# Kernel optimization log

Measured on AMD Instinct MI355X. Metric: run time of the kernel, lower is better.

Reference implementation:

```python
import jax, jax.numpy as jnp
import numpy as np

B, C, T = 128, 295, 2048
D1 = 270
NUM_SUBJECTS = 64

def setup_inputs() -> dict:
    key = jax.random.key(0)
    k_x, k_s, k_w1, k_b1, k_ws = jax.random.split(key, 5)
    X = jax.random.normal(k_x, (B, C, T), dtype=jnp.float32)
    subject_idxs = jax.random.randint(k_s, (B,), 0, NUM_SUBJECTS)
    W1 = jax.random.normal(k_w1, (D1, C), dtype=jnp.float32) * 0.05
    b1 = jax.random.normal(k_b1, (D1,), dtype=jnp.float32) * 0.05
    Ws = jax.random.normal(k_ws, (NUM_SUBJECTS, D1, D1), dtype=jnp.float32) * 0.05
    return {"X": X, "subject_idxs": subject_idxs, "W1": W1, "b1": b1, "Ws": Ws}

def reference(X, subject_idxs, W1, b1, Ws):
    # Shared 1x1 conv: pointwise channel mix C -> D1 with bias.  [B, D1, T]
    y = jnp.einsum('dc,bct->bdt', W1, X) + b1[None, :, None]
    # Top-1 expert dispatch: gather each sample's subject matrix. [B, D1, D1]
    W_sel = Ws[subject_idxs]
    # Per-sample 1x1 conv (batched GEMM), no bias.            [B, D1, T]
    out = jnp.einsum('bed,bdt->bet', W_sel, y)
    return out
```

## Files before the change

kernel.cpp:

```cpp
#include <hip/hip_runtime.h>

#define NSUBJ 64
#define CIN   295
#define DD    270
#define TT    2048
#define BB    128

#define WF_PER_S  92160
#define WF_PER_MT 30720
#define WF_PER_KS 3072
#define WF_PER_KQ 768
#define W1T_PER_KS 10240

typedef __attribute__((ext_vector_type(8))) short bf16x8;
typedef __attribute__((ext_vector_type(4))) float f32x4;
typedef unsigned short u16;

__device__ __forceinline__ u16 f2bf(float f) {
    union { float f; unsigned int u; } v; v.f = f;
    unsigned int r = v.u + 0x7FFFu + ((v.u >> 16) & 1u);
    return (u16)(r >> 16);
}

__device__ __forceinline__ void glds16(const u16* g, u16* lds_base) {
    __builtin_amdgcn_global_load_lds(
        (const __attribute__((address_space(1))) unsigned int*)g,
        (__attribute__((address_space(3))) unsigned int*)lds_base, 16, 0, 0);
}

#define WAITV(N) asm volatile("s_waitcnt vmcnt(" #N ")" ::: "memory")
#define WAITL()  asm volatile("s_waitcnt lgkmcnt(0)" ::: "memory")
#define BAR()    __builtin_amdgcn_s_barrier()
#define SB()     __builtin_amdgcn_sched_barrier(0)

__global__ __launch_bounds__(256) void k_prep_w1(const float* __restrict__ W1,
                                                 const float* __restrict__ b1,
                                                 u16* __restrict__ W1t)
{
    const int idx = blockIdx.x * 256 + threadIdx.x;
    const int ks = idx / W1T_PER_KS;
    const int r  = idx - ks * W1T_PER_KS;
    const int kq = r / 2560;
    const int c  = (r - kq * 2560) >> 3;
    const int k8 = r & 7;
    const int d  = ks * 32 + kq * 8 + k8;
    float v = 0.f;
    if (d < DD) {
        if (c < CIN) v = W1[d * CIN + c];
        else if (c == CIN) v = b1[d];
    }
    W1t[idx] = f2bf(v);
}

__global__ __launch_bounds__(256, 1) void k_fuse_w(const float* __restrict__ Ws,
                                                   const u16* __restrict__ W1t,
                                                   u16* __restrict__ Wf)
{
    __shared__ u16 Aw[3072];
    __shared__ u16 Bw[10240];
    const int tid = threadIdx.x, lane = tid & 63, wid = tid >> 6;
    const int wm = wid >> 1, wn = wid & 1;
    const int mt = blockIdx.x, s = blockIdx.y;
    const int e0 = mt * 96;
    const float* Wsb = Ws + (size_t)s * DD * DD;

    f32x4 acc[3][10];
#pragma unroll
    for (int i = 0; i < 3; ++i)
#pragma unroll
        for (int j = 0; j < 10; ++j) acc[i][j] = (f32x4){0.f, 0.f, 0.f, 0.f};

    for (int ks = 0; ks < 9; ++ks) {
        const int k0 = ks * 32;
#pragma unroll
        for (int ci = 0; ci < 3; ++ci) {
            const int id = tid + ci * 256;
            const int m = id >> 3, q = id & 7;
            const int e = e0 + m, d = k0 + q * 4;
            float2 v01 = {0.f, 0.f}, v23 = {0.f, 0.f};
            if (e < DD) {
                if (d < DD)     v01 = *(const float2*)(Wsb + (size_t)e * DD + d);
                if (d + 2 < DD) v23 = *(const float2*)(Wsb + (size_t)e * DD + d + 2);
            }
            ushort4 h;
            h.x = f2bf(v01.x); h.y = f2bf(v01.y); h.z = f2bf(v23.x); h.w = f2bf(v23.y);
            *(ushort4*)(&Aw[(q >> 1) * 768 + m * 8 + (q & 1) * 4]) = h;
        }
#pragma unroll
        for (int k5 = 0; k5 < 5; ++k5) {
            const int seg = wid * 5 + k5;
            glds16(W1t + (size_t)ks * W1T_PER_KS + seg * 512 + lane * 8, &Bw[seg * 512]);
        }
        __syncthreads();
        bf16x8 af[3];
#pragma unroll
        for (int i = 0; i < 3; ++i)
            af[i] = *(const bf16x8*)(&Aw[(lane >> 4) * 768 + (wm * 48 + i * 16 + (lane & 15)) * 8]);
#pragma unroll
        for (int j = 0; j < 10; ++j) {
            const bf16x8 bfj = *(const bf16x8*)(&Bw[(lane >> 4) * 2560 + (wn * 160 + j * 16 + (lane & 15)) * 8]);
#pragma unroll
            for (int i = 0; i < 3; ++i)
                acc[i][j] = __builtin_amdgcn_mfma_f32_16x16x32_bf16(af[i], bfj, acc[i][j], 0, 0, 0);
        }
        __syncthreads();
    }
    const int rb = (lane >> 4) * 4, cc = lane & 15;
#pragma unroll
    for (int i = 0; i < 3; ++i) {
#pragma unroll
        for (int r = 0; r < 4; ++r) {
            const int e = e0 + wm * 48 + i * 16 + rb + r;
            const int m = e - e0;
#pragma unroll
            for (int j = 0; j < 10; ++j) {
                const int c = wn * 160 + j * 16 + cc;
                Wf[(size_t)s * WF_PER_S + (size_t)mt * WF_PER_MT + (c >> 5) * WF_PER_KS
                   + ((c >> 3) & 3) * WF_PER_KQ + m * 8 + (c & 7)] = f2bf(acc[i][j][r]);
            }
        }
    }
}

__global__ __launch_bounds__(256, 4) void k_main(const float* __restrict__ X,
                                                 const int* __restrict__ subj,
                                                 const u16* __restrict__ Wf,
                                                 float* __restrict__ out)
{
    __shared__ u16 Am[2][3072];
    __shared__ u16 Bm[2][2048];
    const int tid = threadIdx.x, lane = tid & 63, wid = tid >> 6;
    const int wm = wid >> 1, wn = wid & 1;
    const int hw = blockIdx.x;
    const int w  = (hw & 7) * 1536 + (hw >> 3);
    const int b  = w / 96;
    const int r0 = w - b * 96;
    const int nt = r0 / 3, mt = r0 - nt * 3;
    const int t0 = nt * 64;
    const int s = subj[b];
    const float* Xb = X + (size_t)b * CIN * TT;
    const u16* WfA = Wf + (size_t)s * WF_PER_S + (size_t)mt * WF_PER_MT;
    const int bn = tid & 63, bkq = tid >> 6;

    f32x4 acc[3][2];
#pragma unroll
    for (int i = 0; i < 3; ++i)
#pragma unroll
        for (int j = 0; j < 2; ++j) acc[i][j] = (f32x4){0.f, 0.f, 0.f, 0.f};

    float xrE[8], xrO[8];

#define LOADB(KS, XR, CL)                                                   \
    {                                                                       \
        _Pragma("unroll")                                                   \
        for (int q = 0; q < 8; ++q) {                                       \
            const int c = (KS) * 32 + bkq * 8 + q;                          \
            const int cl = ((CL) && c >= CIN) ? (c - 33) : c;               \
            XR[q] = Xb[(size_t)cl * TT + t0 + bn];                          \
        }                                                                   \
    }
#define WRITEB(KS, XR)                                                      \
    {                                                                       \
        bf16x8 h;                                                           \
        _Pragma("unroll")                                                   \
        for (int q = 0; q < 8; ++q) {                                       \
            const int c = (KS) * 32 + bkq * 8 + q;                          \
            u16 v = f2bf(XR[q]);                                            \
            if (c >= CIN) v = (c == CIN) ? (u16)0x3F80 : (u16)0;            \
            h[q] = (short)v;                                                \
        }                                                                   \
        *(bf16x8*)(&Bm[(KS) & 1][bkq * 512 + bn * 8]) = h;                  \
    }
#define STAGEA(KS)                                                          \
    {                                                                       \
        _Pragma("unroll")                                                   \
        for (int k2 = 0; k2 < 2; ++k2) {                                    \
            int seg = wid * 2 + k2;                                         \
            if (seg >= 6) seg -= 6;                                         \
            glds16(WfA + (size_t)(KS) * WF_PER_KS + seg * 512 + lane * 8,   \
                   &Am[(KS) & 1][seg * 512]);                               \
        }                                                                   \
    }
#define COMPUTE(CUR)                                                        \
    {                                                                       \
        bf16x8 bfr[2];                                                      \
        _Pragma("unroll")                                                   \
        for (int j = 0; j < 2; ++j)                                         \
            bfr[j] = *(const bf16x8*)(&Bm[CUR][(lane >> 4) * 512 + (wn * 32 + j * 16 + (lane & 15)) * 8]); \
        _Pragma("unroll")                                                   \
        for (int i = 0; i < 3; ++i) {                                       \
            const bf16x8 af = *(const bf16x8*)(&Am[CUR][(lane >> 4) * 768 + (wm * 48 + i * 16 + (lane & 15)) * 8]); \
            acc[i][0] = __builtin_amdgcn_mfma_f32_16x16x32_bf16(af, bfr[0], acc[i][0], 0, 0, 0); \
            acc[i][1] = __builtin_amdgcn_mfma_f32_16x16x32_bf16(af, bfr[1], acc[i][1], 0, 0, 0); \
        }                                                                   \
    }

    LOADB(0, xrE, 0); SB();
    STAGEA(0);        SB();
    LOADB(1, xrO, 0); SB();
    WAITV(10);
    WRITEB(0, xrE);
    WAITV(8);
    WAITL(); BAR();

#define STEP(KS, XLD, XWR, CL)                                              \
    {                                                                       \
        STAGEA((KS) + 1);         SB();                                     \
        LOADB((KS) + 2, XLD, CL); SB();                                     \
        COMPUTE((KS) & 1);                                                  \
        WAITV(10);                                     \
        WRITEB((KS) + 1, XWR);                                              \
        WAITV(8);                \
        WAITL(); BAR();                                                     \
    }
    for (int kk = 0; kk < 4; ++kk) {
        STEP(2 * kk,     xrE, xrO, 0);
        STEP(2 * kk + 1, xrO, xrE, (2 * kk + 1 == 7));
    }
    STAGEA(9); SB();
    COMPUTE(0);
    WAITV(2);
    WRITEB(9, xrO);
    WAITV(0); WAITL(); BAR();
    COMPUTE(1);

    const int rb = (lane >> 4) * 4, cc = lane & 15;
#pragma unroll
    for (int i = 0; i < 3; ++i) {
#pragma unroll
        for (int r = 0; r < 4; ++r) {
            const int e = mt * 96 + wm * 48 + i * 16 + rb + r;
            if (e < DD) {
#pragma unroll
                for (int j = 0; j < 2; ++j) {
                    const int t = t0 + wn * 32 + j * 16 + cc;
                    out[((size_t)b * DD + e) * TT + t] = acc[i][j][r];
                }
            }
        }
    }
#undef LOADB
#undef WRITEB
#undef STAGEA
#undef COMPUTE
#undef STEP
}

extern "C" void kernel_launch(void* const* d_in, const int* in_sizes, int n_in,
                              void* d_out, int out_size, void* d_ws, size_t ws_size,
                              hipStream_t stream) {
    const float* X    = (const float*)d_in[0];
    const int*   subj = (const int*)d_in[1];
    const float* W1   = (const float*)d_in[2];
    const float* b1   = (const float*)d_in[3];
    const float* Ws   = (const float*)d_in[4];
    float* out = (float*)d_out;

    u16* Wf  = (u16*)d_ws;
    u16* W1t = (u16*)((char*)d_ws + (size_t)NSUBJ * WF_PER_S * 2);

    k_prep_w1<<<dim3(360), 256, 0, stream>>>(W1, b1, W1t);
    k_fuse_w<<<dim3(3, NSUBJ), 256, 0, stream>>>(Ws, W1t, Wf);
    k_main<<<dim3(3 * (TT / 64) * BB), 256, 0, stream>>>(X, subj, Wf, out);
}
```

Before: 211.6 us.

## Triple-buffer A/B LDS stages and deepen prefetch in main GEMM kernel

Moves the k_main pipeline from double to triple buffering. Weight tiles are staged two steps ahead and X rows are loaded three steps ahead, so more global loads are in flight while the MFMAs run. The per-step wait on the A stage is relaxed and the K loop is fully unrolled with rotating register sets. Occupancy hint goes from 4 to 5 blocks and f2bf uses the library conversion. The costs are more LDS per block and more registers, which may block the higher occupancy target, plus added complexity in the vmcnt accounting.

Result: slower. 252.0 us (+19.1%).

```diff
diff --git a/kernel.cpp b/kernel.cpp
--- a/kernel.cpp
+++ b/kernel.cpp
@@ -1,4 +1,5 @@
 #include <hip/hip_runtime.h>
+#include <hip/hip_bf16.h>
 
 #define NSUBJ 64
 #define CIN   295
@@ -17,9 +18,7 @@
 typedef unsigned short u16;
 
 __device__ __forceinline__ u16 f2bf(float f) {
-    union { float f; unsigned int u; } v; v.f = f;
-    unsigned int r = v.u + 0x7FFFu + ((v.u >> 16) & 1u);
-    return (u16)(r >> 16);
+    return __bfloat16_as_ushort(__float2bfloat16(f));
 }
 
 __device__ __forceinline__ void glds16(const u16* g, u16* lds_base) {
@@ -122,13 +121,13 @@
     }
 }
 
-__global__ __launch_bounds__(256, 4) void k_main(const float* __restrict__ X,
+__global__ __launch_bounds__(256, 5) void k_main(const float* __restrict__ X,
                                                  const int* __restrict__ subj,
                                                  const u16* __restrict__ Wf,
                                                  float* __restrict__ out)
 {
-    __shared__ u16 Am[2][3072];
-    __shared__ u16 Bm[2][2048];
+    __shared__ u16 Am[3][3072];
+    __shared__ u16 Bm[3][2048];
     const int tid = threadIdx.x, lane = tid & 63, wid = tid >> 6;
     const int wm = wid >> 1, wn = wid & 1;
     const int hw = blockIdx.x;
@@ -148,7 +147,7 @@
 #pragma unroll
         for (int j = 0; j < 2; ++j) acc[i][j] = (f32x4){0.f, 0.f, 0.f, 0.f};
 
-    float xrE[8], xrO[8];
+    float xr0[8], xr1[8], xr2[8];
 
 #define LOADB(KS, XR, CL)                                                   \
     {                                                                       \
@@ -169,7 +168,7 @@
             if (c >= CIN) v = (c == CIN) ? (u16)0x3F80 : (u16)0;            \
             h[q] = (short)v;                                                \
         }                                                                   \
-        *(bf16x8*)(&Bm[(KS) & 1][bkq * 512 + bn * 8]) = h;                  \
+        *(bf16x8*)(&Bm[(KS) % 3][bkq * 512 + bn * 8]) = h;                  \
     }
 #define STAGEA(KS)                                                          \
     {                                                                       \
@@ -178,7 +177,7 @@
             int seg = wid * 2 + k2;                                         \
             if (seg >= 6) seg -= 6;                                         \
             glds16(WfA + (size_t)(KS) * WF_PER_KS + seg * 512 + lane * 8,   \
-                   &Am[(KS) & 1][seg * 512]);                               \
+                   &Am[(KS) % 3][seg * 512]);                               \
         }                                                                   \
     }
 #define COMPUTE(CUR)                                                        \
@@ -186,43 +185,51 @@
         bf16x8 bfr[2];                                                      \
         _Pragma("unroll")                                                   \
         for (int j = 0; j < 2; ++j)                                         \
-            bfr[j] = *(const bf16x8*)(&Bm[CUR][(lane >> 4) * 512 + (wn * 32 + j * 16 + (lane & 15)) * 8]); \
+            bfr[j] = *(const bf16x8*)(&Bm[(CUR) % 3][(lane >> 4) * 512 + (wn * 32 + j * 16 + (lane & 15)) * 8]); \
         _Pragma("unroll")                                                   \
         for (int i = 0; i < 3; ++i) {                                       \
-            const bf16x8 af = *(const bf16x8*)(&Am[CUR][(lane >> 4) * 768 + (wm * 48 + i * 16 + (lane & 15)) * 8]); \
+            const bf16x8 af = *(const bf16x8*)(&Am[(CUR) % 3][(lane >> 4) * 768 + (wm * 48 + i * 16 + (lane & 15)) * 8]); \
             acc[i][0] = __builtin_amdgcn_mfma_f32_16x16x32_bf16(af, bfr[0], acc[i][0], 0, 0, 0); \
             acc[i][1] = __builtin_amdgcn_mfma_f32_16x16x32_bf16(af, bfr[1], acc[i][1], 0, 0, 0); \
         }                                                                   \
     }
 
-    LOADB(0, xrE, 0); SB();
+    LOADB(0, xr0, 0); SB();
     STAGEA(0);        SB();
-    LOADB(1, xrO, 0); SB();
+    LOADB(1, xr1, 0); SB();
+    STAGEA(1);        SB();
+    LOADB(2, xr2, 0); SB();
+    WAITV(20);
+    WRITEB(0, xr0);
+    WAITV(18);
+    WAITL(); BAR();
+
+#define STEP(KS, XLD, XWR, CL)                                              \
+    {                                                                       \
+        STAGEA((KS) + 2);         SB();                                     \
+        LOADB((KS) + 3, XLD, CL); SB();                                     \
+        COMPUTE(KS);                                                        \
+        WAITV(18);               \
+        WRITEB((KS) + 1, XWR);                                              \
+        WAITL(); BAR();                                                     \
+    }
+    STEP(0, xr0, xr1, 0);
+    STEP(1, xr1, xr2, 0);
+    STEP(2, xr2, xr0, 0);
+    STEP(3, xr0, xr1, 0);
+    STEP(4, xr1, xr2, 0);
+    STEP(5, xr2, xr0, 0);
+    STEP(6, xr0, xr1, 1);
+    STAGEA(9); SB();
+    COMPUTE(7);
     WAITV(10);
-    WRITEB(0, xrE);
-    WAITV(8);
+    WRITEB(8, xr2);
     WAITL(); BAR();
-
-#define STEP(KS, XLD, XWR, CL)                                              \
-    {                                                                       \
-        STAGEA((KS) + 1);         SB();                                     \
-        LOADB((KS) + 2, XLD, CL); SB();                                     \
-        COMPUTE((KS) & 1);                                                  \
-        WAITV(10);                                     \
-        WRITEB((KS) + 1, XWR);                                              \
-        WAITV(8);                \
-        WAITL(); BAR();                                                     \
-    }
-    for (int kk = 0; kk < 4; ++kk) {
-        STEP(2 * kk,     xrE, xrO, 0);
-        STEP(2 * kk + 1, xrO, xrE, (2 * kk + 1 == 7));
-    }
-    STAGEA(9); SB();
-    COMPUTE(0);
-    WAITV(2);
-    WRITEB(9, xrO);
-    WAITV(0); WAITL(); BAR();
-    COMPUTE(1);
+    COMPUTE(8);
+    WAITV(0);
+    WRITEB(9, xr0);
+    WAITL(); BAR();
+    COMPUTE(9);
 
     const int rb = (lane >> 4) * 4, cc = lane & 15;
 #pragma unroll
```
